# Kernel optimization log

Measured on AMD Instinct MI355X. Metric: run time of the kernel, lower is better.

## Reference

```python
import jax, jax.numpy as jnp
import numpy as np

B, K, I, H = 128, 512, 512, 512  # batch, seq_len, input_dim, hidden_dim


def setup_inputs() -> dict:
    key = jax.random.key(0)
    k1, k2, k3, k4, k5 = jax.random.split(key, 5)
    s_i = 1.0 / np.sqrt(H)
    return {
        "visual_seq": jax.random.normal(k1, (B, K, I), dtype=jnp.float32),
        # PyTorch GRU layout: gates stacked [r, z, n] along first dim
        "W_ih": jax.random.uniform(k2, (3 * H, I), minval=-s_i, maxval=s_i, dtype=jnp.float32),
        "W_hh": jax.random.uniform(k3, (3 * H, H), minval=-s_i, maxval=s_i, dtype=jnp.float32),
        "b_ih": jax.random.uniform(k4, (3 * H,), minval=-s_i, maxval=s_i, dtype=jnp.float32),
        "b_hh": jax.random.uniform(k5, (3 * H,), minval=-s_i, maxval=s_i, dtype=jnp.float32),
    }


def reference(visual_seq, W_ih, W_hh, b_ih, b_hh):
    # Fused single-layer GRU over all K steps (equivalent to the per-frame
    # torch loop with zero-initialized hidden state).
    Bs, Ks, _ = visual_seq.shape
    Hs = W_hh.shape[1]
    # Precompute input-gate projections for all timesteps: (K, B, 3H)
    x_gates = jnp.einsum('bki,gi->kbg', visual_seq, W_ih) + b_ih

    def step(h, xg):
        hg = h @ W_hh.T + b_hh                      # (B, 3H)
        xr, xz, xn = jnp.split(xg, 3, axis=-1)
        hr, hz, hn = jnp.split(hg, 3, axis=-1)
        r = jax.nn.sigmoid(xr + hr)
        z = jax.nn.sigmoid(xz + hz)
        n = jnp.tanh(xn + r * hn)
        h_new = (1.0 - z) * n + z * h
        return h_new, None

    h0 = jnp.zeros((Bs, Hs), dtype=visual_seq.dtype)
    h_final, _ = jax.lax.scan(step, h0, x_gates)
    return h_final  # (B, H) == h[-1] in the torch code
```

## Files before the change

### kernel.cpp

```cpp
#include <hip/hip_runtime.h>
#include <hip/hip_bf16.h>


#define CH 32
#define XG_BYTES (CH * 128 * 1536 * 4)
#define HB_BYTES (2 * 128 * 512 * 2)
#define HSTATE_BYTES (128 * 512 * 4)
#define CNT_STRIDE 16
#define CNT_BYTES (512 * 4 * CNT_STRIDE * 4)

typedef float  floatx4 __attribute__((ext_vector_type(4)));
typedef short  shortx8 __attribute__((ext_vector_type(8)));

__device__ __forceinline__ unsigned short f2bf(float f) {
    unsigned int u = __float_as_uint(f);
    u = (u + 0x7FFFu + ((u >> 16) & 1u)) >> 16;
    return (unsigned short)u;
}

__global__ __launch_bounds__(256, 1)
void gru_fused(const float* __restrict__ vis, const float* __restrict__ Wih,
               const float* __restrict__ bih, const float* __restrict__ Whh,
               const float* __restrict__ bhh,
               const float* __restrict__ xgR, float* __restrict__ xgW,
               unsigned short* __restrict__ hb, float* __restrict__ hstate,
               unsigned int* __restrict__ cnt, float* __restrict__ out,
               int kg0, int gemm_kg0, int do_rec, int do_gemm) {
    __shared__ unsigned short Ast[64][40];
    __shared__ unsigned short Bst[64][40];

    const int bx = blockIdx.x;
    const int t = threadIdx.x;
    const int wave = t >> 6, lane = t & 63, quad = lane >> 4, l16 = lane & 15;

    if (do_rec && bx < 64) {
        const int ug = bx & 15, bg = bx >> 4;
        const int u0 = ug * 32, b0 = bg * 32;
        const int mt = wave & 1, u16 = wave >> 1;
        const int b_base = b0 + mt * 16 + quad * 4;
        const int u = u0 + u16 * 16 + l16;

        shortx8 w[3][16];
        #pragma unroll
        for (int g = 0; g < 3; ++g) {
            #pragma unroll
            for (int kt = 0; kt < 16; ++kt) {
                const float* p = Whh + ((size_t)(g * 512 + u)) * 512 + kt * 32 + quad * 8;
                float4 a = *(const float4*)p;
                float4 b = *(const float4*)(p + 4);
                shortx8 v;
                v[0] = (short)f2bf(a.x); v[1] = (short)f2bf(a.y);
                v[2] = (short)f2bf(a.z); v[3] = (short)f2bf(a.w);
                v[4] = (short)f2bf(b.x); v[5] = (short)f2bf(b.y);
                v[6] = (short)f2bf(b.z); v[7] = (short)f2bf(b.w);
                w[g][kt] = v;
            }
        }
        const float bhr = bhh[u], bhz = bhh[512 + u], bhn = bhh[1024 + u];

        float hp[4];
        if (kg0 == 0) {
            hp[0] = hp[1] = hp[2] = hp[3] = 0.f;
        } else {
            #pragma unroll
            for (int reg = 0; reg < 4; ++reg) hp[reg] = hstate[(size_t)(b_base + reg) * 512 + u];
        }

        for (int s = 0; s < CH; ++s) {
            const int kg = kg0 + s;
            float xr[4], xz[4], xn[4];
            #pragma unroll
            for (int reg = 0; reg < 4; ++reg) {
                const float* xgp = xgR + ((size_t)s * 128 + b_base + reg) * 1536 + u;
                xr[reg] = xgp[0]; xz[reg] = xgp[512]; xn[reg] = xgp[1024];
            }

            union { unsigned long long u8[2]; shortx8 v; } af[16];
            if (kg > 0) {
                const unsigned int* fp = cnt + ((size_t)(kg - 1) * 4 + bg) * CNT_STRIDE;
                while (__hip_atomic_load(fp, __ATOMIC_RELAXED, __HIP_MEMORY_SCOPE_AGENT) < 16u)
                    __builtin_amdgcn_s_sleep(1);
                const unsigned short* hsrc = hb + (size_t)((kg - 1) & 1) * (128 * 512)
                                                + (size_t)(b0 + mt * 16 + l16) * 512 + quad * 8;
                #pragma unroll
                for (int kt = 0; kt < 16; ++kt) {
                    af[kt].u8[0] = __hip_atomic_load((const unsigned long long*)(hsrc + kt * 32),
                                                     __ATOMIC_RELAXED, __HIP_MEMORY_SCOPE_AGENT);
                    af[kt].u8[1] = __hip_atomic_load((const unsigned long long*)(hsrc + kt * 32 + 4),
                                                     __ATOMIC_RELAXED, __HIP_MEMORY_SCOPE_AGENT);
                }
            } else {
                #pragma unroll
                for (int kt = 0; kt < 16; ++kt) { af[kt].u8[0] = 0ull; af[kt].u8[1] = 0ull; }
            }

            floatx4 aR = {0,0,0,0}, aZ = {0,0,0,0}, aN = {0,0,0,0};
            #pragma unroll
            for (int kt = 0; kt < 16; ++kt) {
                aR = __builtin_amdgcn_mfma_f32_16x16x32_bf16(af[kt].v, w[0][kt], aR, 0, 0, 0);
                aZ = __builtin_amdgcn_mfma_f32_16x16x32_bf16(af[kt].v, w[1][kt], aZ, 0, 0, 0);
                aN = __builtin_amdgcn_mfma_f32_16x16x32_bf16(af[kt].v, w[2][kt], aN, 0, 0, 0);
            }

            unsigned short* hdst = hb + (size_t)(kg & 1) * (128 * 512);
            #pragma unroll
            for (int reg = 0; reg < 4; ++reg) {
                const float r = 1.f / (1.f + __expf(-(xr[reg] + aR[reg] + bhr)));
                const float z = 1.f / (1.f + __expf(-(xz[reg] + aZ[reg] + bhz)));
                const float n = tanhf(xn[reg] + r * (aN[reg] + bhn));
                const float h = (1.f - z) * n + z * hp[reg];
                hp[reg] = h;
                const float h_odd = __shfl_xor(h, 1);
                if (!(lane & 1)) {
                    unsigned int pk = (unsigned int)f2bf(h) | ((unsigned int)f2bf(h_odd) << 16);
                    __hip_atomic_store((unsigned int*)(hdst + (size_t)(b_base + reg) * 512 + u),
                                       pk, __ATOMIC_RELAXED, __HIP_MEMORY_SCOPE_AGENT);
                }
                if (kg == 511) out[(size_t)(b_base + reg) * 512 + u] = h;
            }
            __syncthreads();
            if (t == 0)
                __hip_atomic_fetch_add(cnt + ((size_t)kg * 4 + bg) * CNT_STRIDE, 1u,
                                       __ATOMIC_RELAXED, __HIP_MEMORY_SCOPE_AGENT);
        }

        #pragma unroll
        for (int reg = 0; reg < 4; ++reg)
            hstate[(size_t)(b_base + reg) * 512 + u] = hp[reg];
        return;
    }

    if (!do_gemm) return;
    const int NG = do_rec ? 192 : 256;
    const int gid = do_rec ? bx - 64 : bx;

    for (int T = gid; T < 1536; T += NG) {
        const int g0 = (T % 24) * 64;
        const int m0 = (T / 24) * 64;
        const int kc = m0 >> 7;
        const int b0 = m0 & 127;
        const int kg = gemm_kg0 + kc;

        floatx4 acc[4] = {{0,0,0,0},{0,0,0,0},{0,0,0,0},{0,0,0,0}};

        for (int ki = 0; ki < 16; ++ki) {
            const int i0 = ki * 32;
            #pragma unroll
            for (int rep = 0; rep < 2; ++rep) {
                const int r = (t >> 3) + rep * 32;
                const int c = (t & 7) * 4;
                float4 av = *(const float4*)(vis + ((size_t)(b0 + r) * 512 + kg) * 512 + i0 + c);
                ushort4 ab; ab.x = f2bf(av.x); ab.y = f2bf(av.y); ab.z = f2bf(av.z); ab.w = f2bf(av.w);
                *(ushort4*)&Ast[r][c] = ab;
                float4 bv = *(const float4*)(Wih + (size_t)(g0 + r) * 512 + i0 + c);
                ushort4 bb; bb.x = f2bf(bv.x); bb.y = f2bf(bv.y); bb.z = f2bf(bv.z); bb.w = f2bf(bv.w);
                *(ushort4*)&Bst[r][c] = bb;
            }
            __syncthreads();
            shortx8 afr = *(const shortx8*)(&Ast[wave * 16 + l16][quad * 8]);
            #pragma unroll
            for (int nb = 0; nb < 4; ++nb) {
                shortx8 bfr = *(const shortx8*)(&Bst[nb * 16 + l16][quad * 8]);
                acc[nb] = __builtin_amdgcn_mfma_f32_16x16x32_bf16(afr, bfr, acc[nb], 0, 0, 0);
            }
            __syncthreads();
        }
        #pragma unroll
        for (int nb = 0; nb < 4; ++nb) {
            const int g = g0 + nb * 16 + l16;
            const float bi = bih[g];
            #pragma unroll
            for (int reg = 0; reg < 4; ++reg) {
                const int m = m0 + wave * 16 + quad * 4 + reg;
                xgW[(size_t)m * 1536 + g] = acc[nb][reg] + bi;
            }
        }
    }
}

extern "C" void kernel_launch(void* const* d_in, const int* in_sizes, int n_in,
                              void* d_out, int out_size, void* d_ws, size_t ws_size,
                              hipStream_t stream) {
    const float* vis = (const float*)d_in[0];
    const float* Wih = (const float*)d_in[1];
    const float* Whh = (const float*)d_in[2];
    const float* bih = (const float*)d_in[3];
    const float* bhh = (const float*)d_in[4];
    float* out = (float*)d_out;

    char* ws = (char*)d_ws;
    float* xg0 = (float*)ws;
    float* xg1 = (float*)(ws + XG_BYTES);
    unsigned short* hb = (unsigned short*)(ws + 2 * XG_BYTES);
    float* hstate = (float*)(ws + 2 * XG_BYTES + HB_BYTES);
    unsigned int* cnt = (unsigned int*)(ws + 2 * XG_BYTES + HB_BYTES + HSTATE_BYTES);

    hipMemsetAsync(cnt, 0, CNT_BYTES, stream);

    float* bufs[2] = {xg0, xg1};

    gru_fused<<<256, 256, 0, stream>>>(vis, Wih, bih, Whh, bhh,
                                       xg0, xg0, hb, hstate, cnt, out,
                                       0, 0, 0, 1);
    for (int i = 0; i < 16; ++i) {
        gru_fused<<<256, 256, 0, stream>>>(vis, Wih, bih, Whh, bhh,
                                           bufs[i & 1], bufs[(i + 1) & 1],
                                           hb, hstate, cnt, out,
                                           i * CH, (i + 1) * CH, 1, (i < 15) ? 1 : 0);
    }
}
```

Before: 3.657 ms.

## Fuse input projection into single persistent recurrent kernel with tagged hidden-state sync

Replaces the chunked design (separate input-GEMM blocks writing gate projections to workspace, 17 launches) with one persistent 64-block kernel. Each step computes its own x·W_ih slice from LDS-resident bf16 W_ih and prefetched visual rows. Hidden state is exchanged through 64-bit words that carry a step tag, replacing the counter-based barrier. The intent is to remove the xg round-trip through memory, the launch overhead and the counter atomics. In exchange, the input projection now sits on the serial critical path of every step, and only 64 CUs are used.

```diff
diff --git a/kernel.cpp b/kernel.cpp
--- a/kernel.cpp
+++ b/kernel.cpp
@@ -1,179 +1,180 @@
 #include <hip/hip_runtime.h>
-#include <hip/hip_bf16.h>
 
 
-#define CH 32
-#define XG_BYTES (CH * 128 * 1536 * 4)
-#define HB_BYTES (2 * 128 * 512 * 2)
-#define HSTATE_BYTES (128 * 512 * 4)
-#define CNT_STRIDE 16
-#define CNT_BYTES (512 * 4 * CNT_STRIDE * 4)
+#define HBT_BYTES (2 * 128 * 256 * 8)
 
 typedef float  floatx4 __attribute__((ext_vector_type(4)));
 typedef short  shortx8 __attribute__((ext_vector_type(8)));
 
 __device__ __forceinline__ unsigned short f2bf(float f) {
-    unsigned int u = __float_as_uint(f);
-    u = (u + 0x7FFFu + ((u >> 16) & 1u)) >> 16;
-    return (unsigned short)u;
+    unsigned int uu = __float_as_uint(f);
+    uu = (uu + 0x7FFFu + ((uu >> 16) & 1u)) >> 16;
+    return (unsigned short)uu;
 }
 
 __global__ __launch_bounds__(256, 1)
-void gru_fused(const float* __restrict__ vis, const float* __restrict__ Wih,
-               const float* __restrict__ bih, const float* __restrict__ Whh,
-               const float* __restrict__ bhh,
-               const float* __restrict__ xgR, float* __restrict__ xgW,
-               unsigned short* __restrict__ hb, float* __restrict__ hstate,
-               unsigned int* __restrict__ cnt, float* __restrict__ out,
-               int kg0, int gemm_kg0, int do_rec, int do_gemm) {
-    __shared__ unsigned short Ast[64][40];
-    __shared__ unsigned short Bst[64][40];
+void gru_rec(const float* __restrict__ vis, const float* __restrict__ Wih,
+             const float* __restrict__ bih, const float* __restrict__ Whh,
+             const float* __restrict__ bhh,
+             unsigned long long* __restrict__ hbt, float* __restrict__ out) {
+    __shared__ unsigned short Wlds[96 * 512];
+    __shared__ unsigned short Vlds[32 * 512];
 
-    const int bx = blockIdx.x;
-    const int t = threadIdx.x;
+    const int bx = blockIdx.x, t = threadIdx.x;
     const int wave = t >> 6, lane = t & 63, quad = lane >> 4, l16 = lane & 15;
+    const int ug = bx & 15, bg = bx >> 4;
+    const int u0 = ug * 32, b0 = bg * 32;
+    const int mt = wave & 1, u16 = wave >> 1;
+    const int b_base = b0 + mt * 16 + quad * 4;
+    const int u = u0 + u16 * 16 + l16;
+    const int rrow = b0 + mt * 16 + l16;
 
-    if (do_rec && bx < 64) {
-        const int ug = bx & 15, bg = bx >> 4;
-        const int u0 = ug * 32, b0 = bg * 32;
-        const int mt = wave & 1, u16 = wave >> 1;
-        const int b_base = b0 + mt * 16 + quad * 4;
-        const int u = u0 + u16 * 16 + l16;
+    shortx8 w[3][16];
+    #pragma unroll
+    for (int g = 0; g < 3; ++g) {
+        #pragma unroll
+        for (int kt = 0; kt < 16; ++kt) {
+            const float* p = Whh + ((size_t)(g * 512 + u)) * 512 + kt * 32 + quad * 8;
+            float4 a = *(const float4*)p;
+            float4 b = *(const float4*)(p + 4);
+            shortx8 v;
+            v[0] = (short)f2bf(a.x); v[1] = (short)f2bf(a.y);
+            v[2] = (short)f2bf(a.z); v[3] = (short)f2bf(a.w);
+            v[4] = (short)f2bf(b.x); v[5] = (short)f2bf(b.y);
+            v[6] = (short)f2bf(b.z); v[7] = (short)f2bf(b.w);
+            w[g][kt] = v;
+        }
+    }
+    const float bhr = bhh[u], bhz = bhh[512 + u], bhn = bhh[1024 + u];
+    const float bir = bih[u], biz = bih[512 + u], bin = bih[1024 + u];
 
-        shortx8 w[3][16];
+    for (int i = t; i < 96 * 128; i += 256) {
+        const int r = i >> 7, cq = i & 127;
+        const int g = r >> 5, lu = r & 31;
+        const float* p = Wih + ((size_t)(g * 512 + u0 + lu)) * 512 + cq * 4;
+        float4 vv = *(const float4*)p;
+        ushort4 b4;
+        b4.x = f2bf(vv.x); b4.y = f2bf(vv.y); b4.z = f2bf(vv.z); b4.w = f2bf(vv.w);
+        *(ushort4*)&Wlds[r * 512 + ((cq * 4) ^ ((r & 7) << 3))] = b4;
+    }
+
+    float hp[4] = {0.f, 0.f, 0.f, 0.f};
+
+    const int vrow = t >> 7;
+    const int vcq = t & 127;
+    float4 S[16];
+    {
+        const float* vp = vis + ((size_t)(b0 + vrow) * 512 + 0) * 512 + vcq * 4;
         #pragma unroll
-        for (int g = 0; g < 3; ++g) {
+        for (int it = 0; it < 16; ++it)
+            S[it] = *(const float4*)(vp + (size_t)it * (2 * 512 * 512));
+    }
+
+    const int ra = mt * 16 + l16, xra = (ra & 7) << 3;
+    const int rb = u16 * 16 + l16, xrb = (rb & 7) << 3;
+
+    for (int kg = 0; kg < 512; ++kg) {
+        __syncthreads();
+        #pragma unroll
+        for (int it = 0; it < 16; ++it) {
+            const int r = vrow + it * 2;
+            ushort4 b4;
+            b4.x = f2bf(S[it].x); b4.y = f2bf(S[it].y);
+            b4.z = f2bf(S[it].z); b4.w = f2bf(S[it].w);
+            *(ushort4*)&Vlds[r * 512 + ((vcq * 4) ^ ((r & 7) << 3))] = b4;
+        }
+        __syncthreads();
+
+        floatx4 xR = {0,0,0,0}, xZ = {0,0,0,0}, xN = {0,0,0,0};
+        #pragma unroll
+        for (int kt = 0; kt < 16; ++kt) {
+            const int co = kt * 32 + quad * 8;
+            shortx8 a  = *(const shortx8*)&Vlds[ra * 512 + (co ^ xra)];
+            shortx8 bR = *(const shortx8*)&Wlds[rb * 512 + (co ^ xrb)];
+            shortx8 bZ = *(const shortx8*)&Wlds[(32 + rb) * 512 + (co ^ xrb)];
+            shortx8 bN = *(const shortx8*)&Wlds[(64 + rb) * 512 + (co ^ xrb)];
+            xR = __builtin_amdgcn_mfma_f32_16x16x32_bf16(a, bR, xR, 0, 0, 0);
+            xZ = __builtin_amdgcn_mfma_f32_16x16x32_bf16(a, bZ, xZ, 0, 0, 0);
+            xN = __builtin_amdgcn_mfma_f32_16x16x32_bf16(a, bN, xN, 0, 0, 0);
+        }
+
+        union LU { unsigned long long v; unsigned int d[2]; };
+        LU L[16][4];
+        if (kg > 0) {
+            const unsigned int expv = (unsigned int)(kg - 1);
+            const size_t pbase = (size_t)((kg - 1) & 1) * 32768;
+            const unsigned long long* sp = hbt + pbase + (size_t)rrow * 256
+                                              + ((lane & 31) >> 1) * 16 + (lane & 1) * 8;
+            for (;;) {
+                unsigned int tg = (unsigned int)(__hip_atomic_load(sp, __ATOMIC_RELAXED,
+                                                 __HIP_MEMORY_SCOPE_AGENT) >> 32);
+                if (__ballot(tg != expv) == 0ull) break;
+                __builtin_amdgcn_s_sleep(1);
+            }
+            const unsigned long long* hbp = hbt + pbase + (size_t)rrow * 256 + quad * 4;
+            for (;;) {
+                #pragma unroll
+                for (int kt = 0; kt < 16; ++kt) {
+                    #pragma unroll
+                    for (int j = 0; j < 4; ++j)
+                        L[kt][j].v = __hip_atomic_load(hbp + kt * 16 + j,
+                                        __ATOMIC_RELAXED, __HIP_MEMORY_SCOPE_AGENT);
+                }
+                unsigned int err = 0u;
+                #pragma unroll
+                for (int kt = 0; kt < 16; ++kt) {
+                    #pragma unroll
+                    for (int j = 0; j < 4; ++j) err |= (L[kt][j].d[1] ^ expv);
+                }
+                if (__ballot(err != 0u) == 0ull) break;
+                __builtin_amdgcn_s_sleep(1);
+            }
+        } else {
             #pragma unroll
             for (int kt = 0; kt < 16; ++kt) {
-                const float* p = Whh + ((size_t)(g * 512 + u)) * 512 + kt * 32 + quad * 8;
-                float4 a = *(const float4*)p;
-                float4 b = *(const float4*)(p + 4);
-                shortx8 v;
-                v[0] = (short)f2bf(a.x); v[1] = (short)f2bf(a.y);
-                v[2] = (short)f2bf(a.z); v[3] = (short)f2bf(a.w);
-                v[4] = (short)f2bf(b.x); v[5] = (short)f2bf(b.y);
-                v[6] = (short)f2bf(b.z); v[7] = (short)f2bf(b.w);
-                w[g][kt] = v;
+                #pragma unroll
+                for (int j = 0; j < 4; ++j) L[kt][j].v = 0ull;
             }
         }
-        const float bhr = bhh[u], bhz = bhh[512 + u], bhn = bhh[1024 + u];
 
-        float hp[4];
-        if (kg0 == 0) {
-            hp[0] = hp[1] = hp[2] = hp[3] = 0.f;
-        } else {
-            #pragma unroll
-            for (int reg = 0; reg < 4; ++reg) hp[reg] = hstate[(size_t)(b_base + reg) * 512 + u];
+        floatx4 aR = {0,0,0,0}, aZ = {0,0,0,0}, aN = {0,0,0,0};
+        #pragma unroll
+        for (int kt = 0; kt < 16; ++kt) {
+            union { unsigned int d[4]; shortx8 v; } af;
+            af.d[0] = L[kt][0].d[0]; af.d[1] = L[kt][1].d[0];
+            af.d[2] = L[kt][2].d[0]; af.d[3] = L[kt][3].d[0];
+            aR = __builtin_amdgcn_mfma_f32_16x16x32_bf16(af.v, w[0][kt], aR, 0, 0, 0);
+            aZ = __builtin_amdgcn_mfma_f32_16x16x32_bf16(af.v, w[1][kt], aZ, 0, 0, 0);
+            aN = __builtin_amdgcn_mfma_f32_16x16x32_bf16(af.v, w[2][kt], aN, 0, 0, 0);
         }
 
-        for (int s = 0; s < CH; ++s) {
-            const int kg = kg0 + s;
-            float xr[4], xz[4], xn[4];
+        {
+            const int kn = (kg < 511) ? kg + 1 : 511;
+            const float* vp = vis + ((size_t)(b0 + vrow) * 512 + kn) * 512 + vcq * 4;
             #pragma unroll
-            for (int reg = 0; reg < 4; ++reg) {
-                const float* xgp = xgR + ((size_t)s * 128 + b_base + reg) * 1536 + u;
-                xr[reg] = xgp[0]; xz[reg] = xgp[512]; xn[reg] = xgp[1024];
-            }
-
-            union { unsigned long long u8[2]; shortx8 v; } af[16];
-            if (kg > 0) {
-                const unsigned int* fp = cnt + ((size_t)(kg - 1) * 4 + bg) * CNT_STRIDE;
-                while (__hip_atomic_load(fp, __ATOMIC_RELAXED, __HIP_MEMORY_SCOPE_AGENT) < 16u)
-                    __builtin_amdgcn_s_sleep(1);
-                const unsigned short* hsrc = hb + (size_t)((kg - 1) & 1) * (128 * 512)
-                                                + (size_t)(b0 + mt * 16 + l16) * 512 + quad * 8;
-                #pragma unroll
-                for (int kt = 0; kt < 16; ++kt) {
-                    af[kt].u8[0] = __hip_atomic_load((const unsigned long long*)(hsrc + kt * 32),
-                                                     __ATOMIC_RELAXED, __HIP_MEMORY_SCOPE_AGENT);
-                    af[kt].u8[1] = __hip_atomic_load((const unsigned long long*)(hsrc + kt * 32 + 4),
-                                                     __ATOMIC_RELAXED, __HIP_MEMORY_SCOPE_AGENT);
-                }
-            } else {
-                #pragma unroll
-                for (int kt = 0; kt < 16; ++kt) { af[kt].u8[0] = 0ull; af[kt].u8[1] = 0ull; }
-            }
-
-            floatx4 aR = {0,0,0,0}, aZ = {0,0,0,0}, aN = {0,0,0,0};
-            #pragma unroll
-            for (int kt = 0; kt < 16; ++kt) {
-                aR = __builtin_amdgcn_mfma_f32_16x16x32_bf16(af[kt].v, w[0][kt], aR, 0, 0, 0);
-                aZ = __builtin_amdgcn_mfma_f32_16x16x32_bf16(af[kt].v, w[1][kt], aZ, 0, 0, 0);
-                aN = __builtin_amdgcn_mfma_f32_16x16x32_bf16(af[kt].v, w[2][kt], aN, 0, 0, 0);
-            }
-
-            unsigned short* hdst = hb + (size_t)(kg & 1) * (128 * 512);
-            #pragma unroll
-            for (int reg = 0; reg < 4; ++reg) {
-                const float r = 1.f / (1.f + __expf(-(xr[reg] + aR[reg] + bhr)));
-                const float z = 1.f / (1.f + __expf(-(xz[reg] + aZ[reg] + bhz)));
-                const float n = tanhf(xn[reg] + r * (aN[reg] + bhn));
-                const float h = (1.f - z) * n + z * hp[reg];
-                hp[reg] = h;
-                const float h_odd = __shfl_xor(h, 1);
-                if (!(lane & 1)) {
-                    unsigned int pk = (unsigned int)f2bf(h) | ((unsigned int)f2bf(h_odd) << 16);
-                    __hip_atomic_store((unsigned int*)(hdst + (size_t)(b_base + reg) * 512 + u),
-                                       pk, __ATOMIC_RELAXED, __HIP_MEMORY_SCOPE_AGENT);
-                }
-                if (kg == 511) out[(size_t)(b_base + reg) * 512 + u] = h;
-            }
-            __syncthreads();
-            if (t == 0)
-                __hip_atomic_fetch_add(cnt + ((size_t)kg * 4 + bg) * CNT_STRIDE, 1u,
-                                       __ATOMIC_RELAXED, __HIP_MEMORY_SCOPE_AGENT);
+            for (int it = 0; it < 16; ++it)
+                S[it] = *(const float4*)(vp + (size_t)it * (2 * 512 * 512));
         }
 
+        unsigned long long* hdst = hbt + (size_t)(kg & 1) * 32768;
+        const unsigned long long tagv = ((unsigned long long)(unsigned int)kg) << 32;
         #pragma unroll
-        for (int reg = 0; reg < 4; ++reg)
-            hstate[(size_t)(b_base + reg) * 512 + u] = hp[reg];
-        return;
-    }
-
-    if (!do_gemm) return;
-    const int NG = do_rec ? 192 : 256;
-    const int gid = do_rec ? bx - 64 : bx;
-
-    for (int T = gid; T < 1536; T += NG) {
-        const int g0 = (T % 24) * 64;
-        const int m0 = (T / 24) * 64;
-        const int kc = m0 >> 7;
-        const int b0 = m0 & 127;
-        const int kg = gemm_kg0 + kc;
-
-        floatx4 acc[4] = {{0,0,0,0},{0,0,0,0},{0,0,0,0},{0,0,0,0}};
-
-        for (int ki = 0; ki < 16; ++ki) {
-            const int i0 = ki * 32;
-            #pragma unroll
-            for (int rep = 0; rep < 2; ++rep) {
-                const int r = (t >> 3) + rep * 32;
-                const int c = (t & 7) * 4;
-                float4 av = *(const float4*)(vis + ((size_t)(b0 + r) * 512 + kg) * 512 + i0 + c);
-                ushort4 ab; ab.x = f2bf(av.x); ab.y = f2bf(av.y); ab.z = f2bf(av.z); ab.w = f2bf(av.w);
-                *(ushort4*)&Ast[r][c] = ab;
-                float4 bv = *(const float4*)(Wih + (size_t)(g0 + r) * 512 + i0 + c);
-                ushort4 bb; bb.x = f2bf(bv.x); bb.y = f2bf(bv.y); bb.z = f2bf(bv.z); bb.w = f2bf(bv.w);
-                *(ushort4*)&Bst[r][c] = bb;
+        for (int reg = 0; reg < 4; ++reg) {
+            const float r = 1.f / (1.f + __expf(-(xR[reg] + bir + aR[reg] + bhr)));
+            const float z = 1.f / (1.f + __expf(-(xZ[reg] + biz + aZ[reg] + bhz)));
+            const float nv = xN[reg] + bin + r * (aN[reg] + bhn);
+            const float n = 1.f - 2.f / (__expf(2.f * nv) + 1.f);
+            const float h = (1.f - z) * n + z * hp[reg];
+            hp[reg] = h;
+            const float h_odd = __shfl_xor(h, 1);
+            if (!(lane & 1)) {
+                unsigned long long val = tagv |
+                    (unsigned long long)((unsigned int)f2bf(h) |
+                                         ((unsigned int)f2bf(h_odd) << 16));
+                __hip_atomic_store(hdst + (size_t)(b_base + reg) * 256 + (u >> 1), val,
+                                   __ATOMIC_RELAXED, __HIP_MEMORY_SCOPE_AGENT);
             }
-            __syncthreads();
-            shortx8 afr = *(const shortx8*)(&Ast[wave * 16 + l16][quad * 8]);
-            #pragma unroll
-            for (int nb = 0; nb < 4; ++nb) {
-                shortx8 bfr = *(const shortx8*)(&Bst[nb * 16 + l16][quad * 8]);
-                acc[nb] = __builtin_amdgcn_mfma_f32_16x16x32_bf16(afr, bfr, acc[nb], 0, 0, 0);
-            }
-            __syncthreads();
-        }
-        #pragma unroll
-        for (int nb = 0; nb < 4; ++nb) {
-            const int g = g0 + nb * 16 + l16;
-            const float bi = bih[g];
-            #pragma unroll
-            for (int reg = 0; reg < 4; ++reg) {
-                const int m = m0 + wave * 16 + quad * 4 + reg;
-                xgW[(size_t)m * 1536 + g] = acc[nb][reg] + bi;
-            }
+            if (kg == 511) out[(size_t)(b_base + reg) * 512 + u] = h;
         }
     }
 }
@@ -188,24 +189,9 @@
     const float* bhh = (const float*)d_in[4];
     float* out = (float*)d_out;
 
-    char* ws = (char*)d_ws;
-    float* xg0 = (float*)ws;
-    float* xg1 = (float*)(ws + XG_BYTES);
-    unsigned short* hb = (unsigned short*)(ws + 2 * XG_BYTES);
-    float* hstate = (float*)(ws + 2 * XG_BYTES + HB_BYTES);
-    unsigned int* cnt = (unsigned int*)(ws + 2 * XG_BYTES + HB_BYTES + HSTATE_BYTES);
+    unsigned long long* hbt = (unsigned long long*)d_ws;
 
-    hipMemsetAsync(cnt, 0, CNT_BYTES, stream);
+    hipMemsetAsync(hbt, 0xFF, HBT_BYTES, stream);
 
-    float* bufs[2] = {xg0, xg1};
-
-    gru_fused<<<256, 256, 0, stream>>>(vis, Wih, bih, Whh, bhh,
-                                       xg0, xg0, hb, hstate, cnt, out,
-                                       0, 0, 0, 1);
-    for (int i = 0; i < 16; ++i) {
-        gru_fused<<<256, 256, 0, stream>>>(vis, Wih, bih, Whh, bhh,
-                                           bufs[i & 1], bufs[(i + 1) & 1],
-                                           hb, hstate, cnt, out,
-                                           i * CH, (i + 1) * CH, 1, (i < 15) ? 1 : 0);
-    }
+    gru_rec<<<64, 256, 0, stream>>>(vis, Wih, bih, Whh, bhh, hbt, out);
 }
```

Result: slower. 5.715 ms (+56.3%).
